# Kernel tuning notes

Measured on AMD Instinct MI355X. Metric: run time of the kernel, lower is better.

Reference implementation:

```python
import jax, jax.numpy as jnp
import numpy as np

D = 1024   # cfg.hid (downscaled from 8192)
M = 20000  # cfg.mem_c // 2 (downscaled)
B, LQ = 4, 8
PLAST_S = 0.05
IMPORTANCE = 1.0


def mha_shared_kv(q, kv_k, kv_v, Wi, bi, Wo, bo, nheads):
    """torch nn.MultiheadAttention (batch_first) with batch-shared K/V.
    q: [B,Lq,D]; kv_k/kv_v: [Lk,D] shared across batch (avoids the .repeat()
    materialization in the original torch code while computing identical math)."""
    dh = D // nheads
    Wq, Wk, Wv = jnp.split(Wi, 3, axis=0)
    bq, bk, bv = jnp.split(bi, 3)
    qp = (jnp.einsum('bqd,ed->bqe', q, Wq) + bq) * (dh ** -0.5)
    kp = kv_k @ Wk.T + bk              # [Lk,D]
    vp = kv_v @ Wv.T + bv              # [Lk,D]
    qh = qp.reshape(q.shape[0], q.shape[1], nheads, dh)      # [B,Lq,h,dh]
    kh = kp.reshape(kp.shape[0], nheads, dh)                 # [Lk,h,dh]
    vh = vp.reshape(vp.shape[0], nheads, dh)                 # [Lk,h,dh]
    scores = jnp.einsum('bqhd,khd->bhqk', qh, kh)            # [B,h,Lq,Lk]
    attn = jax.nn.softmax(scores, axis=-1)
    ctx = jnp.einsum('bhqk,khd->bqhd', attn, vh)
    ctx = ctx.reshape(q.shape[0], q.shape[1], D)
    return ctx @ Wo.T + bo


def setup_inputs() -> dict:
    key = jax.random.key(0)
    ks = jax.random.split(key, 16)
    s = 0.02
    return {
        'q':    jax.random.normal(ks[0], (B, LQ, D), jnp.float32),
        'data': jax.random.normal(ks[1], (B, D), jnp.float32),
        'ek':   jax.random.normal(ks[2], (M, D), jnp.float32),
        'ev':   jax.random.normal(ks[3], (M, D), jnp.float32),
        'sk':   jax.random.normal(ks[4], (M, D), jnp.float32),
        'sv':   jax.random.normal(ks[5], (M, D), jnp.float32),
        'wm':   jax.random.normal(ks[6], (10, D), jnp.float32),
        'Wi_e': jax.random.normal(ks[7], (3 * D, D), jnp.float32) * s,
        'bi_e': jnp.zeros((3 * D,), jnp.float32),
        'Wo_e': jax.random.normal(ks[8], (D, D), jnp.float32) * s,
        'bo_e': jnp.zeros((D,), jnp.float32),
        'Wi_s': jax.random.normal(ks[9], (3 * D, D), jnp.float32) * s,
        'bi_s': jnp.zeros((3 * D,), jnp.float32),
        'Wo_s': jax.random.normal(ks[10], (D, D), jnp.float32) * s,
        'bo_s': jnp.zeros((D,), jnp.float32),
        'Wi_w': jax.random.normal(ks[11], (3 * D, D), jnp.float32) * s,
        'bi_w': jnp.zeros((3 * D,), jnp.float32),
        'Wo_w': jax.random.normal(ks[12], (D, D), jnp.float32) * s,
        'bo_w': jnp.zeros((D,), jnp.float32),
        'Wrp':  jax.random.normal(ks[13], (D, 3 * D), jnp.float32) * s,
        'brp':  jnp.zeros((D,), jnp.float32),
        'eu':   jnp.zeros((M,), jnp.float32),
    }


def reference(q, data, ek, ev, sk, sv, wm,
              Wi_e, bi_e, Wo_e, bo_e,
              Wi_s, bi_s, Wo_s, bo_s,
              Wi_w, bi_w, Wo_w, bo_w,
              Wrp, brp, eu):
    # ---- NeuroMemory.read ----
    e_r = mha_shared_kv(q, ek, ev, Wi_e, bi_e, Wo_e, bo_e, 16)
    s_r = mha_shared_kv(q, sk, sv, Wi_s, bi_s, Wo_s, bo_s, 16)
    w_r = mha_shared_kv(q, wm, wm, Wi_w, bi_w, Wo_w, bo_w, 8)
    read_out = jnp.concatenate([e_r, s_r, w_r], axis=-1) @ Wrp.T + brp  # [B,Lq,D]

    # ---- NeuroMemory.write (episodic, Hebbian plasticity update) ----
    scores = data @ ek.T                       # [B,M]
    probs = jax.nn.softmax(scores, axis=-1)    # [B,M]
    upd = probs * (PLAST_S * IMPORTANCE)       # [B,M]
    u = upd.mean(axis=0)[:, None]              # [M,1] (batch-mean update strength)
    d = data.mean(axis=0)[None, :]             # [1,D]
    new_ek = ek * (1.0 - u) + d * u            # [M,D]
    new_ev = ev * (1.0 - u) + d * u            # [M,D]
    new_eu = eu * 0.99 + jax.lax.stop_gradient(probs.sum(axis=0))  # [M]
    return (read_out, new_ek, new_ev, new_eu)
```

## Files before the change

### kernel.cpp

```cpp
#include <hip/hip_runtime.h>
#include <hip/hip_fp16.h>
#include <hip/hip_bf16.h>
#include <cstdint>
#include <cstddef>

#define D_HID 1024
#define MEM_M 20000
#define NBATCH 4
#define BL 32
#define NROWS 512
#define SROWS_E 516
#define SROWS_S 512
#define BK 32
#define LDT 40
#define PV_NC 8

typedef __attribute__((ext_vector_type(8))) short short8;
typedef __attribute__((ext_vector_type(4))) float f32x4;
typedef __attribute__((ext_vector_type(16))) float f32x16;
typedef __attribute__((ext_vector_type(4))) unsigned short us4;

__device__ inline ushort f2bf(float f) {
    __hip_bfloat16 b = __float2bfloat16(f);
    return *reinterpret_cast<ushort*>(&b);
}
__device__ inline float h2f(ushort u) {
    __half h; *reinterpret_cast<ushort*>(&h) = u; return __half2float(h);
}

__device__ __forceinline__ void block_sync_lds() {
    asm volatile("s_waitcnt lgkmcnt(0)" ::: "memory");
    __builtin_amdgcn_s_barrier();
}

struct SkDesc  { const float* A; const float* B; int K; int M; };
struct SkDescs { SkDesc d[5]; };
struct RdDesc  { const float* bias; float* dst; int M; int ldc; float alpha; };
struct RdDescs { RdDesc d[5]; };

__device__ __forceinline__ void skinny_body(const SkDesc dd, float* __restrict__ part,
                                            int gk, int k0, int n0, int tid)
{
    __shared__ float As[32][132];
    __shared__ float Bs[64][129];
    const int K = dd.K, M = dd.M;
    {
        const int r = tid >> 3, cbl = (tid & 7) * 16;
        if (r < M) {
            const float* src = dd.A + (size_t)r * K + k0 + cbl;
            #pragma unroll
            for (int i = 0; i < 4; ++i) {
                const float4 v = *(const float4*)(src + i * 4);
                As[r][cbl + i * 4 + 0] = v.x; As[r][cbl + i * 4 + 1] = v.y;
                As[r][cbl + i * 4 + 2] = v.z; As[r][cbl + i * 4 + 3] = v.w;
            }
        } else {
            #pragma unroll
            for (int i = 0; i < 16; ++i) As[r][cbl + i] = 0.f;
        }
    }
    {
        const int r = tid >> 2, cbl = (tid & 3) * 32;
        const float* src = dd.B + (size_t)(n0 + r) * K + k0 + cbl;
        #pragma unroll
        for (int i = 0; i < 8; ++i) {
            const float4 v = *(const float4*)(src + i * 4);
            Bs[r][cbl + i * 4 + 0] = v.x; Bs[r][cbl + i * 4 + 1] = v.y;
            Bs[r][cbl + i * 4 + 2] = v.z; Bs[r][cbl + i * 4 + 3] = v.w;
        }
    }
    __syncthreads();
    const int n = tid & 63, mg = tid >> 6;
    float acc[8];
    #pragma unroll
    for (int i = 0; i < 8; ++i) acc[i] = 0.f;
    #pragma unroll 4
    for (int k = 0; k < 128; k += 4) {
        const float b0 = Bs[n][k + 0], b1 = Bs[n][k + 1];
        const float b2 = Bs[n][k + 2], b3 = Bs[n][k + 3];
        #pragma unroll
        for (int i = 0; i < 8; ++i) {
            const float4 a = *(const float4*)&As[mg * 8 + i][k];
            acc[i] = fmaf(a.x, b0, fmaf(a.y, b1, fmaf(a.z, b2, fmaf(a.w, b3, acc[i]))));
        }
    }
    #pragma unroll
    for (int i = 0; i < 8; ++i)
        part[((size_t)gk * 32 + mg * 8 + i) * 1024 + n0 + n] = acc[i];
}

__global__ __launch_bounds__(256)
void k_skinny(SkDescs ds, float* __restrict__ part)
{
    skinny_body(ds.d[blockIdx.z], part,
                blockIdx.z * gridDim.y + blockIdx.y,
                blockIdx.y * 128, blockIdx.x * 64, threadIdx.x);
}

__global__ __launch_bounds__(256)
void k_head(SkDescs ds, float* __restrict__ part,
            const float* __restrict__ ek, const float* __restrict__ sk,
            ushort* __restrict__ kvb)
{
    const int bx = blockIdx.x;
    const int tid = threadIdx.x;
    if (bx < 640) {
        const int g = bx >> 7;
        const int rem = bx & 127;
        const int kc = rem >> 4;
        const int n0 = (rem & 15) * 64;
        skinny_body(ds.d[g], part, g * 8 + kc, kc * 128, n0, tid);
    } else {
        const size_t nchunks = (size_t)2 * MEM_M * D_HID / 8;
        for (size_t i = (size_t)(bx - 640) * 256 + tid; i < nchunks;
             i += (size_t)1408 * 256) {
            const size_t base = i * 8;
            const float* src = (base < (size_t)MEM_M * D_HID)
                             ? (ek + base) : (sk + base - (size_t)MEM_M * D_HID);
            const float4 v0 = *(const float4*)(src);
            const float4 v1 = *(const float4*)(src + 4);
            alignas(16) ushort o[8];
            o[0] = f2bf(v0.x); o[1] = f2bf(v0.y); o[2] = f2bf(v0.z); o[3] = f2bf(v0.w);
            o[4] = f2bf(v1.x); o[5] = f2bf(v1.y); o[6] = f2bf(v1.z); o[7] = f2bf(v1.w);
            *(short8*)(kvb + base) = *(const short8*)o;
        }
    }
}

__global__ __launch_bounds__(256)
void k_skred(RdDescs ds, const float* __restrict__ part, int nkc)
{
    const int g = blockIdx.y;
    const int m = blockIdx.x;
    const RdDesc dd = ds.d[g];
    if (m >= dd.M) return;
    const int c = threadIdx.x * 4;
    float4 s = make_float4(0.f, 0.f, 0.f, 0.f);
    for (int kc = 0; kc < nkc; ++kc) {
        const float4 v = *(const float4*)&part[((size_t)(g * nkc + kc) * 32 + m) * 1024 + c];
        s.x += v.x; s.y += v.y; s.z += v.z; s.w += v.w;
    }
    const float4 b = *(const float4*)(dd.bias + c);
    float4 o;
    o.x = (s.x + b.x) * dd.alpha; o.y = (s.y + b.y) * dd.alpha;
    o.z = (s.z + b.z) * dd.alpha; o.w = (s.w + b.w) * dd.alpha;
    *(float4*)(dd.dst + (size_t)m * dd.ldc + c) = o;
}

__global__ __launch_bounds__(256)
void mfma_scores(const ushort* __restrict__ A_e, const ushort* __restrict__ ekb,
                 const ushort* __restrict__ A_s, const ushort* __restrict__ skb,
                 __half* __restrict__ S_e, __half* __restrict__ S_s,
                 const float* __restrict__ c0_e, const float* __restrict__ c0_s)
{
    __shared__ ushort As[2][128][LDT];
    __shared__ ushort Bs[2][128][LDT];
    const int tid = threadIdx.x;
    const int i = blockIdx.x + 9 * blockIdx.y;
    const int xcd = i & 7, idx = i >> 3;
    const int wg = (xcd < 5 ? xcd * 177 : 885 + (xcd - 5) * 176) + idx;
    const int mi = wg % 9, nbk = wg / 9;
    const int bank = (mi >= 5);
    const int m0 = (bank ? (mi - 5) : mi) * 128;
    const int n0 = nbk * 128;
    const ushort* __restrict__ A = bank ? A_s : A_e;
    const ushort* __restrict__ B = bank ? skb : ekb;
    __half* __restrict__ S = bank ? S_s : S_e;
    const float* __restrict__ c0 = bank ? c0_s : c0_e;
    const int Mreal = bank ? SROWS_S : SROWS_E;

    const int wid = tid >> 6, lane = tid & 63;
    const int wr = (wid >> 1) * 64, wc = (wid & 1) * 64;
    const int l31 = lane & 31, l2 = lane >> 5;

    const int srow = tid >> 1;
    const int ac = (tid & 1) * 16;
    int gbrow = n0 + srow; if (gbrow > MEM_M - 1) gbrow = MEM_M - 1;
    const ushort* Ap = A + (size_t)(m0 + srow) * 1024 + ac;
    const ushort* Bp = B + (size_t)gbrow * 1024 + ac;

    f32x16 acc[2][2];
    #pragma unroll
    for (int fm = 0; fm < 2; ++fm)
        #pragma unroll
        for (int fn = 0; fn < 2; ++fn)
            #pragma unroll
            for (int r = 0; r < 16; ++r) acc[fm][fn][r] = 0.f;

    auto MF = [&](int bu) {
        short8 a[2][2], b[2][2];
        #pragma unroll
        for (int f = 0; f < 2; ++f)
            #pragma unroll
            for (int kh = 0; kh < 2; ++kh) {
                a[f][kh] = *(const short8*)&As[bu][wr + f * 32 + l31][kh * 16 + l2 * 8];
                b[f][kh] = *(const short8*)&Bs[bu][wc + f * 32 + l31][kh * 16 + l2 * 8];
            }
        #pragma unroll
        for (int fm = 0; fm < 2; ++fm)
            #pragma unroll
            for (int fn = 0; fn < 2; ++fn)
                #pragma unroll
                for (int kh = 0; kh < 2; ++kh)
                    acc[fm][fn] = __builtin_amdgcn_mfma_f32_32x32x16_bf16(
                        a[fm][kh], b[fn][kh], acc[fm][fn], 0, 0, 0);
    };

    short8 a00, a01, b00, b01;
    short8 a10, a11, b10, b11;

#define SC_LOAD0(KT) { a00 = *(const short8*)(Ap + (KT)); a01 = *(const short8*)(Ap + (KT) + 8); \
                       b00 = *(const short8*)(Bp + (KT)); b01 = *(const short8*)(Bp + (KT) + 8); }
#define SC_LOAD1(KT) { a10 = *(const short8*)(Ap + (KT)); a11 = *(const short8*)(Ap + (KT) + 8); \
                       b10 = *(const short8*)(Bp + (KT)); b11 = *(const short8*)(Bp + (KT) + 8); }
#define SC_STORE0(BU) { *(short8*)&As[BU][srow][ac] = a00; *(short8*)&As[BU][srow][ac + 8] = a01; \
                        *(short8*)&Bs[BU][srow][ac] = b00; *(short8*)&Bs[BU][srow][ac + 8] = b01; }
#define SC_STORE1(BU) { *(short8*)&As[BU][srow][ac] = a10; *(short8*)&As[BU][srow][ac + 8] = a11; \
                        *(short8*)&Bs[BU][srow][ac] = b10; *(short8*)&Bs[BU][srow][ac + 8] = b11; }

    SC_LOAD0(0);
    SC_LOAD1(32);
    SC_STORE0(0);
    block_sync_lds();
    for (int it = 0; it < 16; ++it) {
        const int kt = it * 64;
        if (it < 15) SC_LOAD0(kt + 64);
        MF(0);
        SC_STORE1(1);
        block_sync_lds();
        if (it < 15) SC_LOAD1(kt + 96);
        MF(1);
        if (it < 15) SC_STORE0(0);
        block_sync_lds();
    }
#undef SC_LOAD0
#undef SC_LOAD1
#undef SC_STORE0
#undef SC_STORE1

    #pragma unroll
    for (int fm = 0; fm < 2; ++fm) {
        #pragma unroll
        for (int fn = 0; fn < 2; ++fn) {
            #pragma unroll
            for (int r = 0; r < 16; ++r) {
                const int row = m0 + wr + fm * 32 + (r & 3) + 8 * (r >> 2) + 4 * l2;
                if (row >= Mreal) continue;
                const int col = n0 + wc + fn * 32 + l31;
                if (col < MEM_M)
                    S[(size_t)row * MEM_M + col] = __float2half(acc[fm][fn][r] + c0[row]);
            }
        }
    }
}

__global__ __launch_bounds__(256)
void mfma_pv(const ushort* __restrict__ P_e, const ushort* __restrict__ P_s,
             const float* __restrict__ ev, const float* __restrict__ sv,
             float* __restrict__ part)
{
    __shared__ ushort As[2][128][LDT];
    __shared__ ushort Bs[2][128][LDT];
    const int tid = threadIdx.x;
    const int bid = blockIdx.x + 8 * (blockIdx.y + 4 * blockIdx.z);
    const int wgs = (bid & 7) * 64 + (bid >> 3);
    const int nI = wgs & 7, mI = (wgs >> 3) & 3;
    const int z = wgs >> 5;
    const int bank = z >> 3, c = z & 7;
    const ushort* __restrict__ P = bank ? P_s : P_e;
    const float* __restrict__ V = bank ? sv : ev;
    const int m0 = mI * 128, n0 = nI * 128;
    const int ks0 = (c * 625) / PV_NC, ks1 = ((c + 1) * 625) / PV_NC;
    const int wid = tid >> 6, lane = tid & 63;
    const int wr = (wid >> 1) * 64, wc = (wid & 1) * 64;
    const int l31 = lane & 31, l2 = lane >> 5;
    const int kb = (tid & 7) * 4, nb2 = (tid >> 3) * 4;
    const int srow = tid >> 1, ac = (tid & 1) * 16;
    const ushort* Pp = P + (size_t)(m0 + srow) * MEM_M + ac;

    f32x16 acc[2][2];
    #pragma unroll
    for (int fm = 0; fm < 2; ++fm)
        #pragma unroll
        for (int fn = 0; fn < 2; ++fn)
            #pragma unroll
            for (int r = 0; r < 16; ++r) acc[fm][fn][r] = 0.f;

    auto MF = [&](int bu) {
        short8 a[2][2], b[2][2];
        #pragma unroll
        for (int f = 0; f < 2; ++f)
            #pragma unroll
            for (int kh = 0; kh < 2; ++kh) {
                a[f][kh] = *(const short8*)&As[bu][wr + f * 32 + l31][kh * 16 + l2 * 8];
                b[f][kh] = *(const short8*)&Bs[bu][wc + f * 32 + l31][kh * 16 + l2 * 8];
            }
        #pragma unroll
        for (int fm = 0; fm < 2; ++fm)
            #pragma unroll
            for (int fn = 0; fn < 2; ++fn)
                #pragma unroll
                for (int kh = 0; kh < 2; ++kh)
                    acc[fm][fn] = __builtin_amdgcn_mfma_f32_32x32x16_bf16(
                        a[fm][kh], b[fn][kh], acc[fm][fn], 0, 0, 0);
    };

    short8 pa00, pa01, pa10, pa11;
    float4 q00, q01, q02, q03, q10, q11, q12, q13;

#define PV_LOAD0(T) { const int kt = (T) * 32; \
    pa00 = *(const short8*)(Pp + kt); pa01 = *(const short8*)(Pp + kt + 8); \
    q00 = *(const float4*)(V + (size_t)(kt + kb + 0) * 1024 + n0 + nb2); \
    q01 = *(const float4*)(V + (size_t)(kt + kb + 1) * 1024 + n0 + nb2); \
    q02 = *(const float4*)(V + (size_t)(kt + kb + 2) * 1024 + n0 + nb2); \
    q03 = *(const float4*)(V + (size_t)(kt + kb + 3) * 1024 + n0 + nb2); }
#define PV_LOAD1(T) { const int kt = (T) * 32; \
    pa10 = *(const short8*)(Pp + kt); pa11 = *(const short8*)(Pp + kt + 8); \
    q10 = *(const float4*)(V + (size_t)(kt + kb + 0) * 1024 + n0 + nb2); \
    q11 = *(const float4*)(V + (size_t)(kt + kb + 1) * 1024 + n0 + nb2); \
    q12 = *(const float4*)(V + (size_t)(kt + kb + 2) * 1024 + n0 + nb2); \
    q13 = *(const float4*)(V + (size_t)(kt + kb + 3) * 1024 + n0 + nb2); }
#define PV_STORE0(BU) { \
    *(short8*)&As[BU][srow][ac] = pa00; *(short8*)&As[BU][srow][ac + 8] = pa01; \
    us4 w; \
    w.x = f2bf(q00.x); w.y = f2bf(q01.x); w.z = f2bf(q02.x); w.w = f2bf(q03.x); \
    *(us4*)&Bs[BU][nb2 + 0][kb] = w; \
    w.x = f2bf(q00.y); w.y = f2bf(q01.y); w.z = f2bf(q02.y); w.w = f2bf(q03.y); \
    *(us4*)&Bs[BU][nb2 + 1][kb] = w; \
    w.x = f2bf(q00.z); w.y = f2bf(q01.z); w.z = f2bf(q02.z); w.w = f2bf(q03.z); \
    *(us4*)&Bs[BU][nb2 + 2][kb] = w; \
    w.x = f2bf(q00.w); w.y = f2bf(q01.w); w.z = f2bf(q02.w); w.w = f2bf(q03.w); \
    *(us4*)&Bs[BU][nb2 + 3][kb] = w; }
#define PV_STORE1(BU) { \
    *(short8*)&As[BU][srow][ac] = pa10; *(short8*)&As[BU][srow][ac + 8] = pa11; \
    us4 w; \
    w.x = f2bf(q10.x); w.y = f2bf(q11.x); w.z = f2bf(q12.x); w.w = f2bf(q13.x); \
    *(us4*)&Bs[BU][nb2 + 0][kb] = w; \
    w.x = f2bf(q10.y); w.y = f2bf(q11.y); w.z = f2bf(q12.y); w.w = f2bf(q13.y); \
    *(us4*)&Bs[BU][nb2 + 1][kb] = w; \
    w.x = f2bf(q10.z); w.y = f2bf(q11.z); w.z = f2bf(q12.z); w.w = f2bf(q13.z); \
    *(us4*)&Bs[BU][nb2 + 2][kb] = w; \
    w.x = f2bf(q10.w); w.y = f2bf(q11.w); w.z = f2bf(q12.w); w.w = f2bf(q13.w); \
    *(us4*)&Bs[BU][nb2 + 3][kb] = w; }

    PV_LOAD0(ks0);
    if (ks0 + 1 < ks1) PV_LOAD1(ks0 + 1);
    PV_STORE0(0);
    block_sync_lds();
    for (int t = ks0; t < ks1; t += 2) {
        if (t + 2 < ks1) PV_LOAD0(t + 2);
        MF(0);
        if (t + 1 < ks1) PV_STORE1(1);
        block_sync_lds();
        if (t + 1 < ks1) {
            if (t + 3 < ks1) PV_LOAD1(t + 3);
            MF(1);
            if (t + 2 < ks1) PV_STORE0(0);
            block_sync_lds();
        }
    }
#undef PV_LOAD0
#undef PV_LOAD1
#undef PV_STORE0
#undef PV_STORE1

    float* __restrict__ po = part + (size_t)z * NROWS * 1024;
    #pragma unroll
    for (int fm = 0; fm < 2; ++fm)
        #pragma unroll
        for (int fn = 0; fn < 2; ++fn)
            #pragma unroll
            for (int r = 0; r < 16; ++r) {
                const int row = m0 + wr + fm * 32 + (r & 3) + 8 * (r >> 2) + 4 * l2;
                const int col = n0 + wc + fn * 32 + l31;
                po[(size_t)row * 1024 + col] = acc[fm][fn][r];
            }
}

__global__ __launch_bounds__(256)
void k_T(const float* __restrict__ qp,
         const float* __restrict__ Wi_e, const float* __restrict__ bi_e,
         const float* __restrict__ Wi_s, const float* __restrict__ bi_s,
         ushort* __restrict__ A_e, float* __restrict__ c0_e,
         ushort* __restrict__ A_s, float* __restrict__ c0_s,
         const float* __restrict__ data, float* __restrict__ dmean)
{
    const int bq = blockIdx.x;
    const int tid = threadIdx.x;
    if (bq >= 128) {
        if (bq < 252) {
            const int row = SROWS_E + (bq - 128);
            us4 z4; z4.x = 0; z4.y = 0; z4.z = 0; z4.w = 0;
            *(us4*)(A_e + (size_t)row * 1024 + tid * 4) = z4;
        } else {
            for (int t = tid; t < D_HID; t += 256) {
                float s = 0.f;
                #pragma unroll
                for (int b = 0; b < NBATCH; ++b) s += data[b * D_HID + t];
                dmean[t] = 0.25f * s;
                #pragma unroll
                for (int b = 0; b < NBATCH; ++b)
                    A_e[(size_t)(NROWS + b) * 1024 + t] = f2bf(data[b * D_HID + t]);
            }
            if (tid < NBATCH) c0_e[NROWS + tid] = 0.f;
        }
        return;
    }
    const int bank = bq >> 6;
    const int h = (bq >> 2) & 15;
    const int q4 = bq & 3;
    const float* qpB = qp + (size_t)bank * BL * D_HID;
    const float* Wk = (bank ? Wi_s : Wi_e) + (size_t)D_HID * D_HID;
    const float* bk = (bank ? bi_s : bi_e) + D_HID;
    ushort* T  = bank ? A_s : A_e;
    float* c0 = bank ? c0_s : c0_e;

    __shared__ float qs[32][64];
    for (int i = tid; i < 32 * 64; i += 256) {
        const int r = i >> 6, j = i & 63;
        qs[r][j] = qpB[(size_t)r * D_HID + h * 64 + j];
    }
    __syncthreads();
    const int e = q4 * 256 + tid;
    float acc[32];
    #pragma unroll
    for (int r = 0; r < 32; ++r) acc[r] = 0.f;
    for (int j = 0; j < 64; ++j) {
        const float w = Wk[(size_t)(h * 64 + j) * D_HID + e];
        #pragma unroll
        for (int r = 0; r < 32; ++r) acc[r] = fmaf(qs[r][j], w, acc[r]);
    }
    #pragma unroll
    for (int r = 0; r < 32; ++r) T[(size_t)(r * 16 + h) * 1024 + e] = f2bf(acc[r]);
    if (q4 == 0 && tid < 32) {
        float s = 0.f;
        for (int j = 0; j < 64; ++j) s += qs[tid][j] * bk[h * 64 + j];
        c0[tid * 16 + h] = s;
    }
}

__global__ __launch_bounds__(256)
void k_softmax(__half* __restrict__ S_e, __half* __restrict__ S_s,
               float* __restrict__ mrow, float* __restrict__ lrow)
{
    const int row = blockIdx.x;
    ushort* p = (row < SROWS_E) ? (ushort*)(S_e + (size_t)row * MEM_M)
                                : (ushort*)(S_s + (size_t)(row - SROWS_E) * MEM_M);
    const bool conv = (row < SROWS_E) ? (row < NROWS) : true;
    __shared__ float red_m[256];
    __shared__ float red_l[256];
    const int tid = threadIdx.x;
    float m = -3.0e38f, l = 0.f;
    for (int c = tid; c < MEM_M / 8; c += 256) {
        alignas(16) ushort t[8];
        *(short8*)t = *(const short8*)(p + c * 8);
        float v[8];
        #pragma unroll
        for (int j = 0; j < 8; ++j) v[j] = h2f(t[j]);
        float cm = v[0];
        #pragma unroll
        for (int j = 1; j < 8; ++j) cm = fmaxf(cm, v[j]);
        const float nm = fmaxf(m, cm);
        float s = 0.f;
        #pragma unroll
        for (int j = 0; j < 8; ++j) s += __expf(v[j] - nm);
        l = l * __expf(m - nm) + s;
        m = nm;
    }
    red_m[tid] = m; red_l[tid] = l; __syncthreads();
    for (int s = 128; s > 0; s >>= 1) {
        if (tid < s) {
            const float m2 = fmaxf(red_m[tid], red_m[tid + s]);
            red_l[tid] = red_l[tid] * __expf(red_m[tid] - m2)
                       + red_l[tid + s] * __expf(red_m[tid + s] - m2);
            red_m[tid] = m2;
        }
        __syncthreads();
    }
    const float rm = red_m[0];
    if (conv) {
        for (int c = tid; c < MEM_M / 8; c += 256) {
            alignas(16) ushort t[8];
            *(short8*)t = *(const short8*)(p + c * 8);
            alignas(16) ushort o[8];
            #pragma unroll
            for (int j = 0; j < 8; ++j) o[j] = f2bf(__expf(h2f(t[j]) - rm));
            *(short8*)(p + c * 8) = *(const short8*)o;
        }
    }
    if (tid == 0) { mrow[row] = rm; lrow[row] = red_l[0]; }
}

__global__ __launch_bounds__(256)
void k_uk(const __half* __restrict__ S_e,
          const float* __restrict__ mrow, const float* __restrict__ lrow,
          const float* __restrict__ eu,
          float* __restrict__ u, float* __restrict__ out_eu)
{
    const int k = blockIdx.x * 256 + threadIdx.x;
    if (k >= MEM_M) return;
    float sp = 0.f;
    #pragma unroll
    for (int b = 0; b < NBATCH; ++b) {
        const int row = NROWS + b;
        sp += __expf(__half2float(S_e[(size_t)row * MEM_M + k]) - mrow[row]) / lrow[row];
    }
    u[k] = 0.05f * 0.25f * sp;
    out_eu[k] = eu[k] * 0.99f + sp;
}

__global__ __launch_bounds__(256)
void k_pvred_upd(const float* __restrict__ part, const float* __restrict__ lrow,
                 float* __restrict__ R,
                 const float* __restrict__ ev, const float* __restrict__ u,
                 const float* __restrict__ dmean, float* __restrict__ out_ev)
{
    const int tid = threadIdx.x;
    if (blockIdx.x < 1024) {
        const size_t perb4 = (size_t)NROWS * 1024 / 4;
        const size_t i = (size_t)blockIdx.x * 256 + tid;
        const int bank = i >= perb4;
        const size_t off4 = i - (size_t)bank * perb4;
        const int m = (int)(off4 >> 8);
        const float inv = 1.f / lrow[bank ? (SROWS_E + m) : m];
        const float4* p = (const float4*)part + (size_t)bank * PV_NC * perb4 + off4;
        float4 s = make_float4(0.f, 0.f, 0.f, 0.f);
        #pragma unroll
        for (int c = 0; c < PV_NC; ++c) {
            const float4 v = p[(size_t)c * perb4];
            s.x += v.x; s.y += v.y; s.z += v.z; s.w += v.w;
        }
        s.x *= inv; s.y *= inv; s.z *= inv; s.w *= inv;
        ((float4*)R)[i] = s;
    } else {
        const int bid = blockIdx.x - 1024;
        const size_t n4 = (size_t)MEM_M * D_HID / 4;
        for (size_t i = (size_t)bid * 256 + tid; i < n4; i += (size_t)1024 * 256) {
            const int k = (int)(i >> 8);
            const int c = (int)(i & 255);
            const float uk = u[k];
            const float om = 1.f - uk;
            const float4 dd = ((const float4*)dmean)[c];
            const float4 b = ((const float4*)ev)[i];
            float4 ob;
            ob.x = b.x * om + dd.x * uk; ob.y = b.y * om + dd.y * uk;
            ob.z = b.z * om + dd.z * uk; ob.w = b.w * om + dd.w * uk;
            ((float4*)out_ev)[i] = ob;
        }
    }
}

__global__ __launch_bounds__(256)
void k_tail(const float* __restrict__ R,
            const float* __restrict__ Wi_e, const float* __restrict__ bi_e,
            const float* __restrict__ Wi_s, const float* __restrict__ bi_s,
            float* __restrict__ ctx,
            const float* __restrict__ qp, const float* __restrict__ kpw,
            const float* __restrict__ vpw,
            const float* __restrict__ ek, const float* __restrict__ u,
            const float* __restrict__ dmean, float* __restrict__ out_ek)
{
    __shared__ float sm[12384];
    const int tid = threadIdx.x;
    const int bx = blockIdx.x;
    if (bx < 32) {
        const int bank = bx >> 4;
        const int h = bx & 15;
        const float* Rb = R + (size_t)bank * NROWS * D_HID;
        const float* Wv = (bank ? Wi_s : Wi_e) + (size_t)2 * D_HID * D_HID;
        const float* bv = (bank ? bi_s : bi_e) + 2 * D_HID;
        float* cb = ctx + (size_t)bank * BL * D_HID;
        float (*Rs)[129] = (float(*)[129])sm;
        float (*Ws)[129] = (float(*)[129])(sm + 32 * 129);
        const int j = tid & 63;
        const int g = tid >> 6;
        float acc[8];
        #pragma unroll
        for (int i = 0; i < 8; ++i) acc[i] = 0.f;
        for (int ec = 0; ec < D_HID; ec += 128) {
            for (int i = tid; i < 32 * 128; i += 256) {
                const int r = i >> 7, e = i & 127;
                Rs[r][e] = Rb[(size_t)(r * 16 + h) * D_HID + ec + e];
            }
            for (int i = tid; i < 64 * 128; i += 256) {
                const int r = i >> 7, e = i & 127;
                Ws[r][e] = Wv[(size_t)(h * 64 + r) * D_HID + ec + e];
            }
            __syncthreads();
            for (int e = 0; e < 128; ++e) {
                const float w = Ws[j][e];
                #pragma unroll
                for (int i = 0; i < 8; ++i)
                    acc[i] = fmaf(Rs[g + 4 * i][e], w, acc[i]);
            }
            __syncthreads();
        }
        #pragma unroll
        for (int i = 0; i < 8; ++i) {
            const int bl = g + 4 * i;
            cb[(size_t)bl * D_HID + h * 64 + j] = acc[i] + bv[h * 64 + j];
        }
    } else if (bx < 64) {
        const int bl = bx - 32;
        float* q = sm;
        float (*kp)[1024] = (float(*)[1024])(sm + 1024);
        float (*pp)[10] = (float(*)[10])(sm + 1024 + 10240);
        const float* qrow = qp + (size_t)(2 * BL + bl) * D_HID;
        for (int i = tid; i < D_HID; i += 256) q[i] = qrow[i];
        for (int i = tid; i < 10 * D_HID; i += 256) kp[i >> 10][i & 1023] = kpw[i];
        __syncthreads();
        if (tid < 80) {
            const int h = tid / 10, k = tid % 10;
            float s = 0.f;
            for (int jj = 0; jj < 128; ++jj) s += q[h * 128 + jj] * kp[k][h * 128 + jj];
            pp[h][k] = s;
        }
        __syncthreads();
        if (tid < 8) {
            float m = -3.0e38f;
            for (int k = 0; k < 10; ++k) m = fmaxf(m, pp[tid][k]);
            float e[10]; float l = 0.f;
            for (int k = 0; k < 10; ++k) { e[k] = __expf(pp[tid][k] - m); l += e[k]; }
            const float inv = 1.f / l;
            for (int k = 0; k < 10; ++k) pp[tid][k] = e[k] * inv;
        }
        __syncthreads();
        float* cw = ctx + (size_t)(2 * BL + bl) * D_HID;
        for (int f = tid; f < D_HID; f += 256) {
            const int h = f >> 7;
            float s = 0.f;
            #pragma unroll
            for (int k = 0; k < 10; ++k) s += pp[h][k] * vpw[(size_t)k * D_HID + f];
            cw[f] = s;
        }
    } else {
        const int bid = bx - 64;
        const size_t n4 = (size_t)MEM_M * D_HID / 4;
        for (size_t i = (size_t)bid * 256 + tid; i < n4; i += (size_t)1024 * 256) {
            const int k = (int)(i >> 8);
            const int c = (int)(i & 255);
            const float uk = u[k];
            const float om = 1.f - uk;
            const float4 dd = ((const float4*)dmean)[c];
            const float4 a = ((const float4*)ek)[i];
            float4 oa;
            oa.x = a.x * om + dd.x * uk; oa.y = a.y * om + dd.y * uk;
            oa.z = a.z * om + dd.z * uk; oa.w = a.w * om + dd.w * uk;
            ((float4*)out_ek)[i] = oa;
        }
    }
}

extern "C" void kernel_launch(void* const* d_in, const int* in_sizes, int n_in,
                              void* d_out, int out_size, void* d_ws, size_t ws_size,
                              hipStream_t stream)
{
    (void)in_sizes; (void)n_in; (void)out_size; (void)ws_size;
    const float* q    = (const float*)d_in[0];
    const float* data = (const float*)d_in[1];
    const float* ek   = (const float*)d_in[2];
    const float* ev   = (const float*)d_in[3];
    const float* sk   = (const float*)d_in[4];
    const float* sv   = (const float*)d_in[5];
    const float* wm   = (const float*)d_in[6];
    const float* Wi_e = (const float*)d_in[7];
    const float* bi_e = (const float*)d_in[8];
    const float* Wo_e = (const float*)d_in[9];
    const float* bo_e = (const float*)d_in[10];
    const float* Wi_s = (const float*)d_in[11];
    const float* bi_s = (const float*)d_in[12];
    const float* Wo_s = (const float*)d_in[13];
    const float* bo_s = (const float*)d_in[14];
    const float* Wi_w = (const float*)d_in[15];
    const float* bi_w = (const float*)d_in[16];
    const float* Wo_w = (const float*)d_in[17];
    const float* bo_w = (const float*)d_in[18];
    const float* Wrp  = (const float*)d_in[19];
    const float* brp  = (const float*)d_in[20];
    const float* eu   = (const float*)d_in[21];

    float* out = (float*)d_out;
    float* out_read = out;
    float* out_ek = out + 32768;
    float* out_ev = out_ek + 20480000;
    float* out_eu = out_ev + 20480000;

    float* ws    = (float*)d_ws;
    float* qp    = ws;
    float* A_e   = qp + 98304;
    float* A_s   = A_e + 655360;
    float* c0_e  = A_s + 524288;
    float* c0_s  = c0_e + 640;
    float* dmean = c0_s + 512;
    float* u     = dmean + 1024;
    float* mrow  = u + 20480;
    float* lrow  = mrow + 1032;
    float* kpw   = lrow + 1032;
    float* vpw   = kpw + 10240;
    float* ctx   = vpw + 10240;
    float* cat   = ctx + 98304;
    float* skpart = cat + 98304;
    float* Rbuf  = skpart;

    ushort* A_e16 = (ushort*)A_e;
    ushort* A_s16 = (ushort*)A_s;

    ushort* ekb = (ushort*)out_ek;
    ushort* skb = ekb + (size_t)MEM_M * D_HID;
    float* part = out_ek;
    __half* S_e = (__half*)out_ev;
    __half* S_s = S_e + (size_t)SROWS_E * MEM_M;

    const dim3 b256(256);
    const float sc16 = 0.125f;
    const float sc8  = 0.08838834764831845f;

    SkDescs s1;
    s1.d[0] = {q,  Wi_e,            1024, 32};
    s1.d[1] = {q,  Wi_s,            1024, 32};
    s1.d[2] = {q,  Wi_w,            1024, 32};
    s1.d[3] = {wm, Wi_w + 1048576,  1024, 10};
    s1.d[4] = {wm, Wi_w + 2097152,  1024, 10};
    k_head<<<2048, b256, 0, stream>>>(s1, skpart, ek, sk, ekb);
    RdDescs r1;
    r1.d[0] = {bi_e,        qp,         32, 1024, sc16};
    r1.d[1] = {bi_s,        qp + 32768, 32, 1024, sc16};
    r1.d[2] = {bi_w,        qp + 65536, 32, 1024, sc8};
    r1.d[3] = {bi_w + 1024, kpw,        10, 1024, 1.f};
    r1.d[4] = {bi_w + 2048, vpw,        10, 1024, 1.f};
    k_skred<<<dim3(32, 5), b256, 0, stream>>>(r1, skpart, 8);

    k_T<<<253, b256, 0, stream>>>(qp, Wi_e, bi_e, Wi_s, bi_s,
                                  A_e16, c0_e, A_s16, c0_s, data, dmean);

    mfma_scores<<<dim3(9, 157), b256, 0, stream>>>(A_e16, ekb, A_s16, skb,
                                                   S_e, S_s, c0_e, c0_s);

    k_softmax<<<SROWS_E + SROWS_S, b256, 0, stream>>>(S_e, S_s, mrow, lrow);
    k_uk<<<79, b256, 0, stream>>>(S_e, mrow, lrow, eu, u, out_eu);

    mfma_pv<<<dim3(8, 4, 2 * PV_NC), b256, 0, stream>>>(
        (const ushort*)S_e, (const ushort*)S_s, ev, sv, part);

    k_pvred_upd<<<2048, b256, 0, stream>>>(part, lrow, Rbuf, ev, u, dmean, out_ev);

    k_tail<<<1088, b256, 0, stream>>>(Rbuf, Wi_e, bi_e, Wi_s, bi_s, ctx,
                                      qp, kpw, vpw, ek, u, dmean, out_ek);

    SkDescs s2;
    s2.d[0] = {ctx,         Wo_e, 1024, 32};
    s2.d[1] = {ctx + 32768, Wo_s, 1024, 32};
    s2.d[2] = {ctx + 65536, Wo_w, 1024, 32};
    s2.d[3] = {ctx,         Wo_e, 1024, 32};
    s2.d[4] = {ctx,         Wo_e, 1024, 32};
    k_skinny<<<dim3(16, 8, 3), b256, 0, stream>>>(s2, skpart);
    RdDescs r2;
    r2.d[0] = {bo_e, cat,        32, 3072, 1.f};
    r2.d[1] = {bo_s, cat + 1024, 32, 3072, 1.f};
    r2.d[2] = {bo_w, cat + 2048, 32, 3072, 1.f};
    r2.d[3] = r2.d[0];
    r2.d[4] = r2.d[0];
    k_skred<<<dim3(32, 3), b256, 0, stream>>>(r2, skpart, 8);

    SkDescs s3;
    s3.d[0] = {cat, Wrp, 3072, 32};
    s3.d[1] = s3.d[0]; s3.d[2] = s3.d[0]; s3.d[3] = s3.d[0]; s3.d[4] = s3.d[0];
    k_skinny<<<dim3(16, 24, 1), b256, 0, stream>>>(s3, skpart);
    RdDescs r3;
    r3.d[0] = {brp, out_read, 32, 1024, 1.f};
    r3.d[1] = r3.d[0]; r3.d[2] = r3.d[0]; r3.d[3] = r3.d[0]; r3.d[4] = r3.d[0];
    k_skred<<<dim3(32, 1), b256, 0, stream>>>(r3, skpart, 24);
}
```

Before: 471.8 us.

## Fuse write-path data·ek scores into the bf16 conversion pass

The write-path scores (data @ ek.T) used to be computed as four extra padded rows in the bf16 MFMA scores GEMM, which took a ninth row-tile of 128 rows that was mostly padding. They are now computed in fp32 while ek is converted to bf16 in k_head, reduced across each wavefront and stored as fp16 in a separate buffer. The scores GEMM drops from 9 to 8 row tiles per column block, and the A_e padding and zeroing work in k_T goes away. The conversion loop now processes one row per wave with shuffle reductions, which adds ALU and shuffle work to a memory-bound pass.

```diff
diff --git a/kernel.cpp b/kernel.cpp
--- a/kernel.cpp
+++ b/kernel.cpp
@@ -9,8 +9,6 @@
 #define NBATCH 4
 #define BL 32
 #define NROWS 512
-#define SROWS_E 516
-#define SROWS_S 512
 #define BK 32
 #define LDT 40
 #define PV_NC 8
@@ -100,7 +98,8 @@
 __global__ __launch_bounds__(256)
 void k_head(SkDescs ds, float* __restrict__ part,
             const float* __restrict__ ek, const float* __restrict__ sk,
-            ushort* __restrict__ kvb)
+            ushort* __restrict__ kvb,
+            const float* __restrict__ data, __half* __restrict__ swr)
 {
     const int bx = blockIdx.x;
     const int tid = threadIdx.x;
@@ -111,18 +110,49 @@
         const int n0 = (rem & 15) * 64;
         skinny_body(ds.d[g], part, g * 8 + kc, kc * 128, n0, tid);
     } else {
-        const size_t nchunks = (size_t)2 * MEM_M * D_HID / 8;
-        for (size_t i = (size_t)(bx - 640) * 256 + tid; i < nchunks;
-             i += (size_t)1408 * 256) {
-            const size_t base = i * 8;
-            const float* src = (base < (size_t)MEM_M * D_HID)
-                             ? (ek + base) : (sk + base - (size_t)MEM_M * D_HID);
-            const float4 v0 = *(const float4*)(src);
-            const float4 v1 = *(const float4*)(src + 4);
-            alignas(16) ushort o[8];
-            o[0] = f2bf(v0.x); o[1] = f2bf(v0.y); o[2] = f2bf(v0.z); o[3] = f2bf(v0.w);
-            o[4] = f2bf(v1.x); o[5] = f2bf(v1.y); o[6] = f2bf(v1.z); o[7] = f2bf(v1.w);
-            *(short8*)(kvb + base) = *(const short8*)o;
+        const int lane = tid & 63;
+        const int wv0 = (bx - 640) * 4 + (tid >> 6);
+        const int c16 = lane * 16;
+        float dreg[NBATCH][16];
+        #pragma unroll
+        for (int b = 0; b < NBATCH; ++b)
+            #pragma unroll
+            for (int j = 0; j < 16; j += 4)
+                *(float4*)&dreg[b][j] = *(const float4*)(data + b * D_HID + c16 + j);
+        for (int r = wv0; r < 2 * MEM_M; r += 5632) {
+            const bool eb = (r < MEM_M);
+            const float* src = eb ? (ek + (size_t)r * D_HID + c16)
+                                  : (sk + (size_t)(r - MEM_M) * D_HID + c16);
+            float v[16];
+            #pragma unroll
+            for (int j = 0; j < 16; j += 4)
+                *(float4*)&v[j] = *(const float4*)(src + j);
+            alignas(16) ushort o[16];
+            #pragma unroll
+            for (int j = 0; j < 16; ++j) o[j] = f2bf(v[j]);
+            ushort* dst = kvb + (size_t)r * D_HID + c16;
+            *(short8*)dst       = *(const short8*)&o[0];
+            *(short8*)(dst + 8) = *(const short8*)&o[8];
+            if (eb) {
+                float dp[NBATCH];
+                #pragma unroll
+                for (int b = 0; b < NBATCH; ++b) {
+                    float s = 0.f;
+                    #pragma unroll
+                    for (int j = 0; j < 16; ++j) s = fmaf(dreg[b][j], v[j], s);
+                    dp[b] = s;
+                }
+                #pragma unroll
+                for (int b = 0; b < NBATCH; ++b)
+                    #pragma unroll
+                    for (int off = 32; off > 0; off >>= 1)
+                        dp[b] += __shfl_down(dp[b], off);
+                if (lane == 0) {
+                    #pragma unroll
+                    for (int b = 0; b < NBATCH; ++b)
+                        swr[(size_t)b * MEM_M + r] = __float2half(dp[b]);
+                }
+            }
         }
     }
 }
@@ -156,18 +186,17 @@
     __shared__ ushort As[2][128][LDT];
     __shared__ ushort Bs[2][128][LDT];
     const int tid = threadIdx.x;
-    const int i = blockIdx.x + 9 * blockIdx.y;
+    const int i = blockIdx.x + 8 * blockIdx.y;
     const int xcd = i & 7, idx = i >> 3;
-    const int wg = (xcd < 5 ? xcd * 177 : 885 + (xcd - 5) * 176) + idx;
-    const int mi = wg % 9, nbk = wg / 9;
-    const int bank = (mi >= 5);
-    const int m0 = (bank ? (mi - 5) : mi) * 128;
+    const int wg = xcd * 157 + idx;
+    const int mi = wg & 7, nbk = wg >> 3;
+    const int bank = (mi >= 4);
+    const int m0 = (bank ? (mi - 4) : mi) * 128;
     const int n0 = nbk * 128;
     const ushort* __restrict__ A = bank ? A_s : A_e;
     const ushort* __restrict__ B = bank ? skb : ekb;
     __half* __restrict__ S = bank ? S_s : S_e;
     const float* __restrict__ c0 = bank ? c0_s : c0_e;
-    const int Mreal = bank ? SROWS_S : SROWS_E;
 
     const int wid = tid >> 6, lane = tid & 63;
     const int wr = (wid >> 1) * 64, wc = (wid & 1) * 64;
@@ -245,7 +274,6 @@
             #pragma unroll
             for (int r = 0; r < 16; ++r) {
                 const int row = m0 + wr + fm * 32 + (r & 3) + 8 * (r >> 2) + 4 * l2;
-                if (row >= Mreal) continue;
                 const int col = n0 + wc + fn * 32 + l31;
                 if (col < MEM_M)
                     S[(size_t)row * MEM_M + col] = __float2half(acc[fm][fn][r] + c0[row]);
@@ -388,21 +416,11 @@
     const int bq = blockIdx.x;
     const int tid = threadIdx.x;
     if (bq >= 128) {
-        if (bq < 252) {
-            const int row = SROWS_E + (bq - 128);
-            us4 z4; z4.x = 0; z4.y = 0; z4.z = 0; z4.w = 0;
-            *(us4*)(A_e + (size_t)row * 1024 + tid * 4) = z4;
-        } else {
-            for (int t = tid; t < D_HID; t += 256) {
-                float s = 0.f;
-                #pragma unroll
-                for (int b = 0; b < NBATCH; ++b) s += data[b * D_HID + t];
-                dmean[t] = 0.25f * s;
-                #pragma unroll
-                for (int b = 0; b < NBATCH; ++b)
-                    A_e[(size_t)(NROWS + b) * 1024 + t] = f2bf(data[b * D_HID + t]);
-            }
-            if (tid < NBATCH) c0_e[NROWS + tid] = 0.f;
+        for (int t = tid; t < D_HID; t += 256) {
+            float s = 0.f;
+            #pragma unroll
+            for (int b = 0; b < NBATCH; ++b) s += data[b * D_HID + t];
+            dmean[t] = 0.25f * s;
         }
         return;
     }
@@ -441,12 +459,15 @@
 
 __global__ __launch_bounds__(256)
 void k_softmax(__half* __restrict__ S_e, __half* __restrict__ S_s,
+               __half* __restrict__ swr,
                float* __restrict__ mrow, float* __restrict__ lrow)
 {
     const int row = blockIdx.x;
-    ushort* p = (row < SROWS_E) ? (ushort*)(S_e + (size_t)row * MEM_M)
-                                : (ushort*)(S_s + (size_t)(row - SROWS_E) * MEM_M);
-    const bool conv = (row < SROWS_E) ? (row < NROWS) : true;
+    ushort* p;
+    bool conv;
+    if (row < NROWS)           { p = (ushort*)(S_e + (size_t)row * MEM_M); conv = true; }
+    else if (row < 2 * NROWS)  { p = (ushort*)(S_s + (size_t)(row - NROWS) * MEM_M); conv = true; }
+    else                       { p = (ushort*)(swr + (size_t)(row - 2 * NROWS) * MEM_M); conv = false; }
     __shared__ float red_m[256];
     __shared__ float red_l[256];
     const int tid = threadIdx.x;
@@ -492,7 +513,7 @@
 }
 
 __global__ __launch_bounds__(256)
-void k_uk(const __half* __restrict__ S_e,
+void k_uk(const __half* __restrict__ swr,
           const float* __restrict__ mrow, const float* __restrict__ lrow,
           const float* __restrict__ eu,
           float* __restrict__ u, float* __restrict__ out_eu)
@@ -502,8 +523,8 @@
     float sp = 0.f;
     #pragma unroll
     for (int b = 0; b < NBATCH; ++b) {
-        const int row = NROWS + b;
-        sp += __expf(__half2float(S_e[(size_t)row * MEM_M + k]) - mrow[row]) / lrow[row];
+        const int row = 2 * NROWS + b;
+        sp += __expf(__half2float(swr[(size_t)b * MEM_M + k]) - mrow[row]) / lrow[row];
     }
     u[k] = 0.05f * 0.25f * sp;
     out_eu[k] = eu[k] * 0.99f + sp;
@@ -522,7 +543,7 @@
         const int bank = i >= perb4;
         const size_t off4 = i - (size_t)bank * perb4;
         const int m = (int)(off4 >> 8);
-        const float inv = 1.f / lrow[bank ? (SROWS_E + m) : m];
+        const float inv = 1.f / lrow[bank * NROWS + m];
         const float4* p = (const float4*)part + (size_t)bank * PV_NC * perb4 + off4;
         float4 s = make_float4(0.f, 0.f, 0.f, 0.f);
         #pragma unroll
@@ -701,6 +722,7 @@
     float* cat   = ctx + 98304;
     float* skpart = cat + 98304;
     float* Rbuf  = skpart;
+    __half* swr  = (__half*)(skpart + 1310720);
 
     ushort* A_e16 = (ushort*)A_e;
     ushort* A_s16 = (ushort*)A_s;
@@ -709,7 +731,7 @@
     ushort* skb = ekb + (size_t)MEM_M * D_HID;
     float* part = out_ek;
     __half* S_e = (__half*)out_ev;
-    __half* S_s = S_e + (size_t)SROWS_E * MEM_M;
+    __half* S_s = S_e + (size_t)NROWS * MEM_M;
 
     const dim3 b256(256);
     const float sc16 = 0.125f;
@@ -721,7 +743,7 @@
     s1.d[2] = {q,  Wi_w,            1024, 32};
     s1.d[3] = {wm, Wi_w + 1048576,  1024, 10};
     s1.d[4] = {wm, Wi_w + 2097152,  1024, 10};
-    k_head<<<2048, b256, 0, stream>>>(s1, skpart, ek, sk, ekb);
+    k_head<<<2048, b256, 0, stream>>>(s1, skpart, ek, sk, ekb, data, swr);
     RdDescs r1;
     r1.d[0] = {bi_e,        qp,         32, 1024, sc16};
     r1.d[1] = {bi_s,        qp + 32768, 32, 1024, sc16};
@@ -730,14 +752,14 @@
     r1.d[4] = {bi_w + 2048, vpw,        10, 1024, 1.f};
     k_skred<<<dim3(32, 5), b256, 0, stream>>>(r1, skpart, 8);
 
-    k_T<<<253, b256, 0, stream>>>(qp, Wi_e, bi_e, Wi_s, bi_s,
+    k_T<<<129, b256, 0, stream>>>(qp, Wi_e, bi_e, Wi_s, bi_s,
                                   A_e16, c0_e, A_s16, c0_s, data, dmean);
 
-    mfma_scores<<<dim3(9, 157), b256, 0, stream>>>(A_e16, ekb, A_s16, skb,
+    mfma_scores<<<dim3(8, 157), b256, 0, stream>>>(A_e16, ekb, A_s16, skb,
                                                    S_e, S_s, c0_e, c0_s);
 
-    k_softmax<<<SROWS_E + SROWS_S, b256, 0, stream>>>(S_e, S_s, mrow, lrow);
-    k_uk<<<79, b256, 0, stream>>>(S_e, mrow, lrow, eu, u, out_eu);
+    k_softmax<<<2 * NROWS + NBATCH, b256, 0, stream>>>(S_e, S_s, swr, mrow, lrow);
+    k_uk<<<79, b256, 0, stream>>>(swr, mrow, lrow, eu, u, out_eu);
 
     mfma_pv<<<dim3(8, 4, 2 * PV_NC), b256, 0, stream>>>(
         (const ushort*)S_e, (const ushort*)S_s, ev, sv, part);
```

New measurement: 456.8 us. -3.2%, faster.
